# Optimization experiments

Hardware: AMD Instinct MI355X
Metric: run time of the kernel (lower is better)

The kernel has to match this reference:

```python
import jax, jax.numpy as jnp
import numpy as np

EPS = 1e-7  # eps used inside bbox_iou
LAMBDA_BBOX = 1.0
LAMBDA_CLS = 1.0


def _coords(b):
    x, y, w, h = b[..., 0], b[..., 1], b[..., 2], b[..., 3]
    return x - w / 2, y - h / 2, x + w / 2, y + h / 2


def _pairwise_giou_loss(pred, target):
    # pred [B,T,4] -> [B,T,1,4]; target [B,O,4] -> [B,1,O,4]; broadcast to [B,T,O]
    b1x1, b1y1, b1x2, b1y2 = _coords(pred[:, :, None, :])
    b2x1, b2y1, b2x2, b2y2 = _coords(target[:, None, :, :])
    w1, h1 = b1x2 - b1x1, b1y2 - b1y1 + EPS
    w2, h2 = b2x2 - b2x1, b2y2 - b2y1 + EPS
    inter = jnp.clip(jnp.minimum(b1x2, b2x2) - jnp.maximum(b1x1, b2x1), 0) * \
            jnp.clip(jnp.minimum(b1y2, b2y2) - jnp.maximum(b1y1, b2y1), 0)
    union = w1 * h1 + w2 * h2 - inter + EPS
    iou = inter / union
    cw = jnp.maximum(b1x2, b2x2) - jnp.minimum(b1x1, b2x1)
    ch = jnp.maximum(b1y2, b2y2) - jnp.minimum(b1y1, b2y1)
    c_area = cw * ch + EPS
    giou = iou - (c_area - union) / c_area
    return 1.0 - giou  # [B,T,O]


def _lsa_rows(c):
    # Jonker-Volgenant shortest augmenting path (same algorithm as scipy's
    # linear_sum_assignment). c is [n, m] with n <= m; returns col4row [n].
    n, m = c.shape
    u = np.zeros(n)
    v = np.zeros(m)
    col4row = np.full(n, -1, np.int64)
    row4col = np.full(m, -1, np.int64)
    for cur in range(n):
        shortest = np.full(m, np.inf)
        path = np.full(m, -1, np.int64)
        SR = np.zeros(n, bool)
        SC = np.zeros(m, bool)
        min_val = 0.0
        i = cur
        sink = -1
        while sink == -1:
            SR[i] = True
            r = min_val + c[i] - u[i] - v
            upd = (~SC) & (r < shortest)
            shortest[upd] = r[upd]
            path[upd] = i
            masked = np.where(SC, np.inf, shortest)
            j = int(np.argmin(masked))
            min_val = masked[j]
            SC[j] = True
            if row4col[j] == -1:
                sink = j
            else:
                i = row4col[j]
        u[cur] += min_val
        sr = SR.copy(); sr[cur] = False
        u[sr] += min_val - shortest[col4row[sr]]
        v[SC] -= min_val - shortest[SC]
        j = sink
        while True:
            i = path[j]
            row4col[j] = i
            col4row[i], j = j, col4row[i]
            if i == cur:
                break
    return col4row


def _hungarian_np(cost):
    # Host callback; sequential per-batch like the original scipy loop.
    cost = np.asarray(cost, np.float64)
    B, T, O = cost.shape
    pred_idx = np.zeros((B, O), np.int32)
    tgt_idx = np.zeros((B, O), np.int32)
    for b in range(B):
        col4row = _lsa_rows(cost[b].T)  # assign each target (O rows) a token
        order = np.argsort(col4row)      # sort by pred index like scipy output
        pred_idx[b] = col4row[order].astype(np.int32)
        tgt_idx[b] = order.astype(np.int32)
    return pred_idx, tgt_idx


def _cost_matrix(pred_bboxes, target_bboxes, pred_classes, target_classes):
    B, T, C = pred_classes.shape
    O = target_classes.shape[1]
    log_probs = jax.nn.log_softmax(pred_classes, axis=-1)              # [B,T,C]
    idx = jnp.broadcast_to(target_classes[:, None, :], (B, T, O))      # [B,T,O]
    cls_neg_log = -jnp.take_along_axis(log_probs, idx, axis=-1)        # [B,T,O]
    ciou_loss = _pairwise_giou_loss(pred_bboxes, target_bboxes)        # [B,T,O]
    return LAMBDA_BBOX * ciou_loss + LAMBDA_CLS * cls_neg_log


def setup_inputs() -> dict:
    key = jax.random.key(0)
    k1, k2, k3, k4 = jax.random.split(key, 4)
    B, T, O, C = 32, 2048, 128, 80
    return {
        "pred_bboxes": jax.random.uniform(k1, (B, T, 4), dtype=jnp.float32),
        "target_bboxes": jax.random.uniform(k2, (B, O, 4), dtype=jnp.float32),
        "pred_classes": jax.random.normal(k3, (B, T, C), dtype=jnp.float32),
        "target_classes": jax.random.randint(k4, (B, O), 0, C, dtype=jnp.int32),
    }


def reference(pred_bboxes, target_bboxes, pred_classes, target_classes):
    cost = _cost_matrix(pred_bboxes, target_bboxes, pred_classes, target_classes)
    B, _, O = cost.shape
    out_spec = (jax.ShapeDtypeStruct((B, O), jnp.int32),
                jax.ShapeDtypeStruct((B, O), jnp.int32))
    pred_idx, tgt_idx = jax.pure_callback(_hungarian_np, out_spec, cost)
    return pred_idx, tgt_idx
```

## Files before the change

kernel.cpp:

```cpp
#include <hip/hip_runtime.h>
#include <math.h>
#include <float.h>

#define BB 32
#define TT 2048
#define OO 128
#define CC 80
#define EPSF 1e-7f
#define NT 256
#define SLOTS 8
#define CPAD 84

struct alignas(16) URow { double u; int row; int pad; };
struct alignas(8)  P2   { int i; int j; };
struct alignas(16) Cand { double v; int j; int pad; };

template<int CTRL>
__device__ __forceinline__ void dpp_lexmin(double& bv, int& bj) {
    int lo = __double2loint(bv), hi = __double2hiint(bv);
    int tlo = __builtin_amdgcn_update_dpp(0, lo, CTRL, 0xF, 0xF, false);
    int thi = __builtin_amdgcn_update_dpp(0x7FF00000, hi, CTRL, 0xF, 0xF, false);
    int tj  = __builtin_amdgcn_update_dpp(0x7FFFFFFF, bj, CTRL, 0xF, 0xF, false);
    double tv = __hiloint2double(thi, tlo);
    if (tv <= bv) { bv = tv; bj = tj; }
}

__global__ __launch_bounds__(NT) void cost_fused_kernel(
    const float* __restrict__ pb, const float* __restrict__ tb,
    const float* __restrict__ cls, const int* __restrict__ tcls,
    float* __restrict__ cost, unsigned long long* __restrict__ rowminarg) {
#pragma clang fp contract(off)
    int b = blockIdx.y;
    int t0 = blockIdx.x * NT;
    int tid = threadIdx.x;

    __shared__ float s_xv[NT * CPAD];
    __shared__ float s_x1[OO], s_y1[OO], s_x2[OO], s_y2[OO], s_w2h2[OO];
    __shared__ int s_tc[OO];

    const float* cbase = cls + ((size_t)b * TT + t0) * CC;
    #pragma unroll
    for (int k = 0; k < CC / 4; ++k) {
        int idx4 = (k * NT + tid) * 4;
        float4 vv = *(const float4*)(cbase + idx4);
        int r = idx4 / CC;
        int c = idx4 - r * CC;
        *(float4*)(&s_xv[r * CPAD + c]) = vv;
    }
    if (tid < OO) {
        float4 tbox = ((const float4*)tb)[b * OO + tid];
        float x1 = tbox.x - tbox.z / 2.f;
        float y1 = tbox.y - tbox.w / 2.f;
        float x2 = tbox.x + tbox.z / 2.f;
        float y2 = tbox.y + tbox.w / 2.f;
        s_x1[tid] = x1; s_y1[tid] = y1; s_x2[tid] = x2; s_y2[tid] = y2;
        float w2 = x2 - x1;
        float h2 = (y2 - y1) + EPSF;
        s_w2h2[tid] = w2 * h2;
        s_tc[tid] = tcls[b * OO + tid];
    }
    __syncthreads();

    size_t bt = (size_t)b * TT + t0 + tid;
    float4 pbox = ((const float4*)pb)[bt];
    float b1x1 = pbox.x - pbox.z / 2.f;
    float b1y1 = pbox.y - pbox.w / 2.f;
    float b1x2 = pbox.x + pbox.z / 2.f;
    float b1y2 = pbox.y + pbox.w / 2.f;
    float w1 = b1x2 - b1x1;
    float h1 = (b1y2 - b1y1) + EPSF;
    float w1h1 = w1 * h1;

    const float* xr = &s_xv[tid * CPAD];
    float m = xr[0];
    #pragma unroll
    for (int c = 1; c < CC; ++c) m = fmaxf(m, xr[c]);
    float ssum = 0.f;
    #pragma unroll
    for (int c = 0; c < CC; ++c) ssum += expf(xr[c] - m);
    float ls = logf(ssum);

    float* cbt = cost + (size_t)b * OO * TT + t0;
    for (int o = 0; o < OO; ++o) {
        float b2x1 = s_x1[o], b2y1 = s_y1[o], b2x2 = s_x2[o], b2y2 = s_y2[o];
        float iw = fminf(b1x2, b2x2) - fmaxf(b1x1, b2x1);
        float ih = fminf(b1y2, b2y2) - fmaxf(b1y1, b2y1);
        iw = fmaxf(iw, 0.f);
        ih = fmaxf(ih, 0.f);
        float inter = iw * ih;
        float uni = ((w1h1 + s_w2h2[o]) - inter) + EPSF;
        float iou = inter / uni;
        float cw = fmaxf(b1x2, b2x2) - fminf(b1x1, b2x1);
        float ch = fmaxf(b1y2, b2y2) - fminf(b1y1, b2y1);
        float c_area = (cw * ch) + EPSF;
        float giou = iou - (c_area - uni) / c_area;
        float bbox_loss = 1.0f - giou;

        float xc = xr[s_tc[o]];
        float shifted = xc - m;
        float cls_neg = -(shifted - ls);

        float cval = bbox_loss + cls_neg;
        cbt[(size_t)o * TT + tid] = cval;

        unsigned long long kv =
            ((unsigned long long)__float_as_uint(cval) << 32)
            | (unsigned long long)(unsigned)(t0 + tid);
        #pragma unroll
        for (int off = 1; off < 64; off <<= 1) {
            unsigned long long o2 = __shfl_xor(kv, off);
            kv = (o2 < kv) ? o2 : kv;
        }
        if ((tid & 63) == 0) atomicMin(&rowminarg[b * OO + o], kv);
    }
}

__global__ __launch_bounds__(NT) void lsa_kernel(
    const float* __restrict__ cost,
    const unsigned long long* __restrict__ rowminarg,
    int* __restrict__ out) {
#pragma clang fp contract(off)
    int b = blockIdx.x;
    int tid = threadIdx.x;
    int lane = tid & 63;
    int wave = tid >> 6;

    __shared__ URow sh_urow[TT];
    __shared__ P2   sh_path2[TT];
    __shared__ int  sh_row4col[TT];
    __shared__ int  sh_claim[TT];
    __shared__ int  sh_col4row[OO];
    __shared__ double sh_u[OO];
    __shared__ int  sh_amin[OO];
    __shared__ int  sh_flag[OO];
    __shared__ int  sh_freelist[OO];
    __shared__ int  sh_selj[OO + 8];
    __shared__ double sh_selm[OO + 8];
    __shared__ int  sh_selrow[OO + 8];
    __shared__ Cand sh_cand[2][4];
    __shared__ int  sh_nfree;

    const float* cb = cost + (size_t)b * OO * TT;
    const int jbase = tid * SLOTS;

    double v_[SLOTS];
    double key[SLOTS];
    #pragma unroll
    for (int s = 0; s < SLOTS; ++s) v_[s] = 0.0;

    if (tid < OO) {
        unsigned long long kv = rowminarg[b * OO + tid];
        sh_u[tid] = (double)__uint_as_float((unsigned)(kv >> 32));
        sh_amin[tid] = (int)(kv & 0xFFFFFFFFull);
        sh_col4row[tid] = -1;
    }
    for (int j = tid; j < TT; j += NT) { sh_row4col[j] = -1; sh_claim[j] = 0x7FFFFFFF; }
    __syncthreads();

    if (tid < OO) atomicMin(&sh_claim[sh_amin[tid]], tid);
    __syncthreads();
    if (tid < OO) {
        int j = sh_amin[tid];
        if (sh_claim[j] == tid) { sh_col4row[tid] = j; sh_row4col[j] = tid; }
    }
    __syncthreads();

    for (int j = tid; j < TT; j += NT) {
        int r = sh_row4col[j];
        URow t; t.row = r; t.u = (r >= 0) ? sh_u[r] : 0.0; t.pad = 0;
        sh_urow[j] = t;
    }
    if (tid < OO) sh_flag[tid] = (sh_col4row[tid] < 0) ? 1 : 0;
    __syncthreads();
    if (tid < OO && sh_flag[tid]) {
        int rank = 0;
        for (int o = 0; o < tid; ++o) rank += sh_flag[o];
        sh_freelist[rank] = tid;
    }
    if (tid == 0) {
        int nf = 0;
        for (int o = 0; o < OO; ++o) nf += sh_flag[o];
        sh_nfree = nf;
    }
    __syncthreads();
    int nfree = sh_nfree;

    int par = 0;
    for (int fi = 0; fi < nfree; ++fi) {
        int cur = sh_freelist[fi];

        #pragma unroll
        for (int s = 0; s < SLOTS; ++s) key[s] = INFINITY;
        int selbits = 0;
        double mv = 0.0;
        int i = cur, jc = -1;
        double ui = sh_u[cur];
        const float* crow0 = cb + (size_t)i * TT + jbase;
        float4 c0 = *(const float4*)crow0;
        float4 c1 = *(const float4*)(crow0 + 4);
        int L = 0, sink;

        while (true) {
            float cv[SLOTS] = {c0.x, c0.y, c0.z, c0.w, c1.x, c1.y, c1.z, c1.w};

            double bv = INFINITY;
            int bj = TT;
            #pragma unroll
            for (int s = 0; s < SLOTS; ++s) {
                if (!((selbits >> s) & 1)) {
                    double r = ((mv + (double)cv[s]) - ui) - v_[s];
                    if (r < key[s]) {
                        key[s] = r;
                        P2 p; p.i = i; p.j = jc;
                        sh_path2[s * NT + tid] = p;
                    }
                    double kk = key[s];
                    if (kk < bv) { bv = kk; bj = jbase + s; }
                }
            }
            dpp_lexmin<0x111>(bv, bj);
            dpp_lexmin<0x112>(bv, bj);
            dpp_lexmin<0x114>(bv, bj);
            dpp_lexmin<0x118>(bv, bj);
            dpp_lexmin<0x142>(bv, bj);
            dpp_lexmin<0x143>(bv, bj);
            int rlo = __builtin_amdgcn_readlane(__double2loint(bv), 63);
            int rhi = __builtin_amdgcn_readlane(__double2hiint(bv), 63);
            double wv = __hiloint2double(rhi, rlo);
            int wj = __builtin_amdgcn_readlane(bj, 63);

            par ^= 1;
            if (lane == 0) {
                Cand c; c.v = wv; c.j = wj; c.pad = 0;
                sh_cand[par][wave] = c;
            }
            __syncthreads();

            Cand cc = sh_cand[par][0];
            double MV = cc.v; int BJ = cc.j;
            #pragma unroll
            for (int w = 1; w < 4; ++w) {
                Cand c2 = sh_cand[par][w];
                if (c2.v < MV || (c2.v == MV && c2.j < BJ)) { MV = c2.v; BJ = c2.j; }
            }
            mv = MV;
            if ((BJ >> 3) == tid) selbits |= 1 << (BJ & 7);
            if (tid == 0) sh_selj[L] = BJ;

            URow ur = sh_urow[BJ];
            if (ur.row < 0) { sink = BJ; break; }
            if (tid == 0) { sh_selm[L] = MV; sh_selrow[L] = ur.row; }
            i = ur.row; ui = ur.u; jc = BJ;
            L++;
            const float* crow = cb + (size_t)i * TT + jbase;
            c0 = *(const float4*)crow;
            c1 = *(const float4*)(crow + 4);
        }

        double M = mv;
        #pragma unroll
        for (int s = 0; s < SLOTS; ++s)
            if ((selbits >> s) & 1) v_[s] = v_[s] - (M - key[s]);
        for (int k = tid; k < L; k += NT)
            sh_u[sh_selrow[k]] = sh_u[sh_selrow[k]] + (M - sh_selm[k]);
        if (tid == 0) {
            sh_u[cur] = sh_u[cur] + M;
            int j = sink;
            while (true) {
                P2 p = sh_path2[(j & 7) * NT + (j >> 3)];
                int ii = p.i;
                sh_row4col[j] = ii;
                sh_col4row[ii] = j;
                if (ii == cur) break;
                j = p.j;
            }
        }
        __syncthreads();
        if (tid <= L) {
            int j = sh_selj[tid];
            int r = sh_row4col[j];
            URow t; t.u = sh_u[r]; t.row = r; t.pad = 0;
            sh_urow[j] = t;
        }
        __syncthreads();
    }

    if (tid < OO) {
        int my = sh_col4row[tid];
        int rank = 0;
        for (int o = 0; o < OO; ++o) rank += (sh_col4row[o] < my) ? 1 : 0;
        out[(size_t)b * OO + rank] = my;
        out[(size_t)(BB + b) * OO + rank] = tid;
    }
}

extern "C" void kernel_launch(void* const* d_in, const int* in_sizes, int n_in,
                              void* d_out, int out_size, void* d_ws, size_t ws_size,
                              hipStream_t stream) {
    const float* pred_bboxes = (const float*)d_in[0];
    const float* target_bboxes = (const float*)d_in[1];
    const float* pred_classes = (const float*)d_in[2];
    const int* target_classes = (const int*)d_in[3];
    int* out = (int*)d_out;

    float* cost = (float*)d_ws;
    unsigned long long* rowminarg =
        (unsigned long long*)(cost + (size_t)BB * OO * TT);

    hipMemsetAsync(rowminarg, 0xFF, (size_t)BB * OO * 8, stream);

    dim3 cgrid(TT / NT, BB);
    cost_fused_kernel<<<cgrid, NT, 0, stream>>>(pred_bboxes, target_bboxes,
                                                pred_classes, target_classes,
                                                cost, rowminarg);
    lsa_kernel<<<BB, NT, 0, stream>>>(cost, rowminarg, out);
}
```

Baseline: 291.9 us.

## Add auction-style augmenting row reduction before shortest-path LSA and drop atomic rowmin

Adds an augmenting row reduction phase, as in Jonker-Volgenant, that processes free rows from a queue. For each row it finds the best and second-best reduced cost with DPP top-2 reductions, then reassigns the column and lowers its price. The goal is to leave fewer unassigned rows for the expensive sequential shortest-augmenting-path loop. The cost kernel now writes per-tile row minima to a buffer instead of using global atomicMin, which removes the memset launch. The risks are extra barriers per ARR step, capped at 256 steps, and the possibility that the dual variables (u, v) no longer match the later phase's invariants.

Result: slower. 328.0 us (+12.4%).

```diff
diff --git a/kernel.cpp b/kernel.cpp
--- a/kernel.cpp
+++ b/kernel.cpp
@@ -10,10 +10,13 @@
 #define NT 256
 #define SLOTS 8
 #define CPAD 84
+#define NTILE 8
+#define ARR_CAP 256
 
 struct alignas(16) URow { double u; int row; int pad; };
 struct alignas(8)  P2   { int i; int j; };
 struct alignas(16) Cand { double v; int j; int pad; };
+struct alignas(16) A3   { double m1; double m2; int j1; int pad; };
 
 template<int CTRL>
 __device__ __forceinline__ void dpp_lexmin(double& bv, int& bj) {
@@ -25,18 +28,48 @@
     if (tv <= bv) { bv = tv; bj = tj; }
 }
 
+template<int CTRL>
+__device__ __forceinline__ void dpp_lexmin_f32(float& bv, int& bj) {
+    int tlo = __builtin_amdgcn_update_dpp(0x7F800000, __float_as_int(bv), CTRL, 0xF, 0xF, false);
+    int tj  = __builtin_amdgcn_update_dpp(0x7FFFFFFF, bj, CTRL, 0xF, 0xF, false);
+    float tv = __int_as_float(tlo);
+    if (tv < bv || (tv == bv && tj < bj)) { bv = tv; bj = tj; }
+}
+
+template<int CTRL>
+__device__ __forceinline__ void dpp_top2(double& m1, int& j1, double& m2) {
+    int a1lo = __double2loint(m1), a1hi = __double2hiint(m1);
+    int a2lo = __double2loint(m2), a2hi = __double2hiint(m2);
+    int b1lo = __builtin_amdgcn_update_dpp(0, a1lo, CTRL, 0xF, 0xF, false);
+    int b1hi = __builtin_amdgcn_update_dpp(0x7FF00000, a1hi, CTRL, 0xF, 0xF, false);
+    int bj   = __builtin_amdgcn_update_dpp(0x7FFFFFFF, j1, CTRL, 0xF, 0xF, false);
+    int b2lo = __builtin_amdgcn_update_dpp(0, a2lo, CTRL, 0xF, 0xF, false);
+    int b2hi = __builtin_amdgcn_update_dpp(0x7FF00000, a2hi, CTRL, 0xF, 0xF, false);
+    double om1 = __hiloint2double(b1hi, b1lo);
+    double om2 = __hiloint2double(b2hi, b2lo);
+    bool w = (om1 < m1) || (om1 == m1 && bj < j1);
+    double lose1 = w ? m1 : om1;
+    double keep2 = w ? om2 : m2;
+    if (w) { m1 = om1; j1 = bj; }
+    m2 = (lose1 < keep2) ? lose1 : keep2;
+}
+
 __global__ __launch_bounds__(NT) void cost_fused_kernel(
     const float* __restrict__ pb, const float* __restrict__ tb,
     const float* __restrict__ cls, const int* __restrict__ tcls,
-    float* __restrict__ cost, unsigned long long* __restrict__ rowminarg) {
+    float* __restrict__ cost, unsigned long long* __restrict__ rowmins) {
 #pragma clang fp contract(off)
     int b = blockIdx.y;
-    int t0 = blockIdx.x * NT;
+    int tile = blockIdx.x;
+    int t0 = tile * NT;
     int tid = threadIdx.x;
+    int lane = tid & 63;
+    int wave = tid >> 6;
 
     __shared__ float s_xv[NT * CPAD];
     __shared__ float s_x1[OO], s_y1[OO], s_x2[OO], s_y2[OO], s_w2h2[OO];
     __shared__ int s_tc[OO];
+    __shared__ unsigned long long s_rmin[OO * 4];
 
     const float* cbase = cls + ((size_t)b * TT + t0) * CC;
     #pragma unroll
@@ -103,21 +136,33 @@
         float cval = bbox_loss + cls_neg;
         cbt[(size_t)o * TT + tid] = cval;
 
-        unsigned long long kv =
-            ((unsigned long long)__float_as_uint(cval) << 32)
-            | (unsigned long long)(unsigned)(t0 + tid);
-        #pragma unroll
-        for (int off = 1; off < 64; off <<= 1) {
-            unsigned long long o2 = __shfl_xor(kv, off);
-            kv = (o2 < kv) ? o2 : kv;
-        }
-        if ((tid & 63) == 0) atomicMin(&rowminarg[b * OO + o], kv);
+        float bvv = cval;
+        int bjj = t0 + tid;
+        dpp_lexmin_f32<0x111>(bvv, bjj);
+        dpp_lexmin_f32<0x112>(bvv, bjj);
+        dpp_lexmin_f32<0x114>(bvv, bjj);
+        dpp_lexmin_f32<0x118>(bvv, bjj);
+        dpp_lexmin_f32<0x142>(bvv, bjj);
+        dpp_lexmin_f32<0x143>(bvv, bjj);
+        if (lane == 63)
+            s_rmin[o * 4 + wave] =
+                ((unsigned long long)__float_as_uint(bvv) << 32) | (unsigned)bjj;
+    }
+    __syncthreads();
+    if (tid < OO) {
+        unsigned long long r0 = s_rmin[tid * 4 + 0];
+        unsigned long long r1 = s_rmin[tid * 4 + 1];
+        unsigned long long r2 = s_rmin[tid * 4 + 2];
+        unsigned long long r3 = s_rmin[tid * 4 + 3];
+        unsigned long long m01 = r0 < r1 ? r0 : r1;
+        unsigned long long m23 = r2 < r3 ? r2 : r3;
+        rowmins[((size_t)b * NTILE + tile) * OO + tid] = m01 < m23 ? m01 : m23;
     }
 }
 
 __global__ __launch_bounds__(NT) void lsa_kernel(
     const float* __restrict__ cost,
-    const unsigned long long* __restrict__ rowminarg,
+    const unsigned long long* __restrict__ rowmins,
     int* __restrict__ out) {
 #pragma clang fp contract(off)
     int b = blockIdx.x;
@@ -133,12 +178,15 @@
     __shared__ double sh_u[OO];
     __shared__ int  sh_amin[OO];
     __shared__ int  sh_flag[OO];
+    __shared__ int  sh_q[OO + ARR_CAP + 16];
     __shared__ int  sh_freelist[OO];
     __shared__ int  sh_selj[OO + 8];
     __shared__ double sh_selm[OO + 8];
     __shared__ int  sh_selrow[OO + 8];
     __shared__ Cand sh_cand[2][4];
+    __shared__ A3   sh_arr[4];
     __shared__ int  sh_nfree;
+    __shared__ int  sh_qt;
 
     const float* cb = cost + (size_t)b * OO * TT;
     const int jbase = tid * SLOTS;
@@ -149,9 +197,15 @@
     for (int s = 0; s < SLOTS; ++s) v_[s] = 0.0;
 
     if (tid < OO) {
-        unsigned long long kv = rowminarg[b * OO + tid];
-        sh_u[tid] = (double)__uint_as_float((unsigned)(kv >> 32));
-        sh_amin[tid] = (int)(kv & 0xFFFFFFFFull);
+        const unsigned long long* p = rowmins + (size_t)b * NTILE * OO + tid;
+        unsigned long long best = p[0];
+        #pragma unroll
+        for (int t = 1; t < NTILE; ++t) {
+            unsigned long long x = p[t * OO];
+            if (x < best) best = x;
+        }
+        sh_u[tid] = (double)__uint_as_float((unsigned)(best >> 32));
+        sh_amin[tid] = (int)(best & 0xFFFFFFFFull);
         sh_col4row[tid] = -1;
     }
     for (int j = tid; j < TT; j += NT) { sh_row4col[j] = -1; sh_claim[j] = 0x7FFFFFFF; }
@@ -162,8 +216,83 @@
     if (tid < OO) {
         int j = sh_amin[tid];
         if (sh_claim[j] == tid) { sh_col4row[tid] = j; sh_row4col[j] = tid; }
-    }
-    __syncthreads();
+        sh_flag[tid] = (sh_col4row[tid] < 0) ? 1 : 0;
+    }
+    __syncthreads();
+    if (tid < OO && sh_flag[tid]) {
+        int rank = 0;
+        for (int o = 0; o < tid; ++o) rank += sh_flag[o];
+        sh_q[rank] = tid;
+    }
+    if (tid == 0) {
+        int nf = 0;
+        for (int o = 0; o < OO; ++o) nf += sh_flag[o];
+        sh_qt = nf;
+    }
+    __syncthreads();
+
+    int qh = 0, qt = sh_qt, steps = 0;
+    while (qh < qt && steps < ARR_CAP) {
+        int i = sh_q[qh];
+        const float* crow = cb + (size_t)i * TT + jbase;
+        float4 c0 = *(const float4*)crow;
+        float4 c1 = *(const float4*)(crow + 4);
+        float cv[SLOTS] = {c0.x, c0.y, c0.z, c0.w, c1.x, c1.y, c1.z, c1.w};
+        double m1 = INFINITY, m2 = INFINITY;
+        int j1 = 0x7FFFFFFF;
+        #pragma unroll
+        for (int s = 0; s < SLOTS; ++s) {
+            double r = (double)cv[s] - v_[s];
+            bool lt = (r < m1);
+            double lose = lt ? m1 : r;
+            if (lt) { m1 = r; j1 = jbase + s; }
+            if (lose < m2) m2 = lose;
+        }
+        dpp_top2<0x111>(m1, j1, m2);
+        dpp_top2<0x112>(m1, j1, m2);
+        dpp_top2<0x114>(m1, j1, m2);
+        dpp_top2<0x118>(m1, j1, m2);
+        dpp_top2<0x142>(m1, j1, m2);
+        dpp_top2<0x143>(m1, j1, m2);
+        if (lane == 63) { A3 a; a.m1 = m1; a.m2 = m2; a.j1 = j1; a.pad = 0; sh_arr[wave] = a; }
+        __syncthreads();
+
+        A3 a0 = sh_arr[0];
+        double U1 = a0.m1, U2 = a0.m2;
+        int J1 = a0.j1;
+        #pragma unroll
+        for (int w = 1; w < 4; ++w) {
+            A3 aw = sh_arr[w];
+            bool wn = (aw.m1 < U1) || (aw.m1 == U1 && aw.j1 < J1);
+            double lose1 = wn ? U1 : aw.m1;
+            double keep2 = wn ? aw.m2 : U2;
+            if (wn) { U1 = aw.m1; J1 = aw.j1; }
+            U2 = (lose1 < keep2) ? lose1 : keep2;
+        }
+        qh++; steps++;
+        if (U1 < U2) {
+            if ((J1 >> 3) == tid) {
+                double d = U2 - U1;
+                int sl = J1 & 7;
+                #pragma unroll
+                for (int ss = 0; ss < SLOTS; ++ss)
+                    if (ss == sl) v_[ss] = v_[ss] - d;
+            }
+            if (tid == 0) {
+                int k = sh_row4col[J1];
+                sh_row4col[J1] = i;
+                sh_col4row[i] = J1;
+                sh_u[i] = U2;
+                int nqt = qt;
+                if (k >= 0) { sh_col4row[k] = -1; sh_q[qt] = k; nqt = qt + 1; }
+                sh_qt = nqt;
+            }
+        } else {
+            if (tid == 0) sh_qt = qt;
+        }
+        __syncthreads();
+        qt = sh_qt;
+    }
 
     for (int j = tid; j < TT; j += NT) {
         int r = sh_row4col[j];
@@ -304,14 +433,12 @@
     int* out = (int*)d_out;
 
     float* cost = (float*)d_ws;
-    unsigned long long* rowminarg =
+    unsigned long long* rowmins =
         (unsigned long long*)(cost + (size_t)BB * OO * TT);
 
-    hipMemsetAsync(rowminarg, 0xFF, (size_t)BB * OO * 8, stream);
-
-    dim3 cgrid(TT / NT, BB);
+    dim3 cgrid(NTILE, BB);
     cost_fused_kernel<<<cgrid, NT, 0, stream>>>(pred_bboxes, target_bboxes,
                                                 pred_classes, target_classes,
-                                                cost, rowminarg);
-    lsa_kernel<<<BB, NT, 0, stream>>>(cost, rowminarg, out);
-}
+                                                cost, rowmins);
+    lsa_kernel<<<BB, NT, 0, stream>>>(cost, rowmins, out);
+}
```

## Fuse cost and assignment kernels with per-batch arrival counter handoff

Applied to the files above, without the earlier changes.

Merges the cost-matrix kernel and the Hungarian solver into one launch. Tile-0 blocks spin on a per-batch atomic counter until all eight tiles of that batch have written their cost slices, then run the assignment solver. Row-min reduction now uses float DPP plus a shared-memory combine and writes per-tile minima instead of 64-bit global atomicMin, which removes the memset of the rowmin buffer. The goal is to save a launch boundary and let early batches start solving while others are still computing. The spin-wait depends on all producer blocks being scheduled and adds a shared-memory union sized by the larger phase.

Result: no change. 295.6 us (+1.3%).

```diff
diff --git a/kernel.cpp b/kernel.cpp
--- a/kernel.cpp
+++ b/kernel.cpp
@@ -10,6 +10,7 @@
 #define NT 256
 #define SLOTS 8
 #define CPAD 84
+#define NTILE 8
 
 struct alignas(16) URow { double u; int row; int pad; };
 struct alignas(8)  P2   { int i; int j; };
@@ -25,120 +26,159 @@
     if (tv <= bv) { bv = tv; bj = tj; }
 }
 
-__global__ __launch_bounds__(NT) void cost_fused_kernel(
+template<int CTRL>
+__device__ __forceinline__ void dpp_lexmin_f32(float& bv, int& bj) {
+    int tlo = __builtin_amdgcn_update_dpp(0x7F800000, __float_as_int(bv), CTRL, 0xF, 0xF, false);
+    int tj  = __builtin_amdgcn_update_dpp(0x7FFFFFFF, bj, CTRL, 0xF, 0xF, false);
+    float tv = __int_as_float(tlo);
+    if (tv < bv || (tv == bv && tj < bj)) { bv = tv; bj = tj; }
+}
+
+union SM {
+    struct {
+        float xv[NT * CPAD];
+        float x1[OO], y1[OO], x2[OO], y2[OO], w2h2[OO];
+        int   tc[OO];
+        unsigned long long rmin[OO * 4];
+    } c;
+    struct {
+        URow   urow[TT];
+        P2     path2[TT];
+        int    row4col[TT];
+        int    claim[TT];
+        int    col4row[OO];
+        double u[OO];
+        int    amin[OO];
+        int    flag[OO];
+        int    freelist[OO];
+        int    selj[OO + 8];
+        double selm[OO + 8];
+        int    selrow[OO + 8];
+        Cand   cand[2][4];
+        int    nfree;
+    } l;
+};
+
+__global__ __launch_bounds__(NT) void hung_fused_kernel(
     const float* __restrict__ pb, const float* __restrict__ tb,
     const float* __restrict__ cls, const int* __restrict__ tcls,
-    float* __restrict__ cost, unsigned long long* __restrict__ rowminarg) {
+    float* __restrict__ cost, unsigned long long* __restrict__ rowmins,
+    int* __restrict__ cnt, int* __restrict__ out) {
 #pragma clang fp contract(off)
-    int b = blockIdx.y;
-    int t0 = blockIdx.x * NT;
-    int tid = threadIdx.x;
-
-    __shared__ float s_xv[NT * CPAD];
-    __shared__ float s_x1[OO], s_y1[OO], s_x2[OO], s_y2[OO], s_w2h2[OO];
-    __shared__ int s_tc[OO];
-
-    const float* cbase = cls + ((size_t)b * TT + t0) * CC;
-    #pragma unroll
-    for (int k = 0; k < CC / 4; ++k) {
-        int idx4 = (k * NT + tid) * 4;
-        float4 vv = *(const float4*)(cbase + idx4);
-        int r = idx4 / CC;
-        int c = idx4 - r * CC;
-        *(float4*)(&s_xv[r * CPAD + c]) = vv;
-    }
-    if (tid < OO) {
-        float4 tbox = ((const float4*)tb)[b * OO + tid];
-        float x1 = tbox.x - tbox.z / 2.f;
-        float y1 = tbox.y - tbox.w / 2.f;
-        float x2 = tbox.x + tbox.z / 2.f;
-        float y2 = tbox.y + tbox.w / 2.f;
-        s_x1[tid] = x1; s_y1[tid] = y1; s_x2[tid] = x2; s_y2[tid] = y2;
-        float w2 = x2 - x1;
-        float h2 = (y2 - y1) + EPSF;
-        s_w2h2[tid] = w2 * h2;
-        s_tc[tid] = tcls[b * OO + tid];
-    }
-    __syncthreads();
-
-    size_t bt = (size_t)b * TT + t0 + tid;
-    float4 pbox = ((const float4*)pb)[bt];
-    float b1x1 = pbox.x - pbox.z / 2.f;
-    float b1y1 = pbox.y - pbox.w / 2.f;
-    float b1x2 = pbox.x + pbox.z / 2.f;
-    float b1y2 = pbox.y + pbox.w / 2.f;
-    float w1 = b1x2 - b1x1;
-    float h1 = (b1y2 - b1y1) + EPSF;
-    float w1h1 = w1 * h1;
-
-    const float* xr = &s_xv[tid * CPAD];
-    float m = xr[0];
-    #pragma unroll
-    for (int c = 1; c < CC; ++c) m = fmaxf(m, xr[c]);
-    float ssum = 0.f;
-    #pragma unroll
-    for (int c = 0; c < CC; ++c) ssum += expf(xr[c] - m);
-    float ls = logf(ssum);
-
-    float* cbt = cost + (size_t)b * OO * TT + t0;
-    for (int o = 0; o < OO; ++o) {
-        float b2x1 = s_x1[o], b2y1 = s_y1[o], b2x2 = s_x2[o], b2y2 = s_y2[o];
-        float iw = fminf(b1x2, b2x2) - fmaxf(b1x1, b2x1);
-        float ih = fminf(b1y2, b2y2) - fmaxf(b1y1, b2y1);
-        iw = fmaxf(iw, 0.f);
-        ih = fmaxf(ih, 0.f);
-        float inter = iw * ih;
-        float uni = ((w1h1 + s_w2h2[o]) - inter) + EPSF;
-        float iou = inter / uni;
-        float cw = fmaxf(b1x2, b2x2) - fminf(b1x1, b2x1);
-        float ch = fmaxf(b1y2, b2y2) - fminf(b1y1, b2y1);
-        float c_area = (cw * ch) + EPSF;
-        float giou = iou - (c_area - uni) / c_area;
-        float bbox_loss = 1.0f - giou;
-
-        float xc = xr[s_tc[o]];
-        float shifted = xc - m;
-        float cls_neg = -(shifted - ls);
-
-        float cval = bbox_loss + cls_neg;
-        cbt[(size_t)o * TT + tid] = cval;
-
-        unsigned long long kv =
-            ((unsigned long long)__float_as_uint(cval) << 32)
-            | (unsigned long long)(unsigned)(t0 + tid);
-        #pragma unroll
-        for (int off = 1; off < 64; off <<= 1) {
-            unsigned long long o2 = __shfl_xor(kv, off);
-            kv = (o2 < kv) ? o2 : kv;
-        }
-        if ((tid & 63) == 0) atomicMin(&rowminarg[b * OO + o], kv);
-    }
-}
-
-__global__ __launch_bounds__(NT) void lsa_kernel(
-    const float* __restrict__ cost,
-    const unsigned long long* __restrict__ rowminarg,
-    int* __restrict__ out) {
-#pragma clang fp contract(off)
-    int b = blockIdx.x;
+    __shared__ SM sm;
+
+    int bx = blockIdx.x;
+    int b = bx >> 3;
+    int tile = bx & 7;
+    int t0 = tile * NT;
     int tid = threadIdx.x;
     int lane = tid & 63;
     int wave = tid >> 6;
 
-    __shared__ URow sh_urow[TT];
-    __shared__ P2   sh_path2[TT];
-    __shared__ int  sh_row4col[TT];
-    __shared__ int  sh_claim[TT];
-    __shared__ int  sh_col4row[OO];
-    __shared__ double sh_u[OO];
-    __shared__ int  sh_amin[OO];
-    __shared__ int  sh_flag[OO];
-    __shared__ int  sh_freelist[OO];
-    __shared__ int  sh_selj[OO + 8];
-    __shared__ double sh_selm[OO + 8];
-    __shared__ int  sh_selrow[OO + 8];
-    __shared__ Cand sh_cand[2][4];
-    __shared__ int  sh_nfree;
+    {
+        const float* cbase = cls + ((size_t)b * TT + t0) * CC;
+        #pragma unroll
+        for (int k = 0; k < CC / 4; ++k) {
+            int idx4 = (k * NT + tid) * 4;
+            float4 vv = *(const float4*)(cbase + idx4);
+            int r = idx4 / CC;
+            int c = idx4 - r * CC;
+            *(float4*)(&sm.c.xv[r * CPAD + c]) = vv;
+        }
+        if (tid < OO) {
+            float4 tbox = ((const float4*)tb)[b * OO + tid];
+            float x1 = tbox.x - tbox.z / 2.f;
+            float y1 = tbox.y - tbox.w / 2.f;
+            float x2 = tbox.x + tbox.z / 2.f;
+            float y2 = tbox.y + tbox.w / 2.f;
+            sm.c.x1[tid] = x1; sm.c.y1[tid] = y1;
+            sm.c.x2[tid] = x2; sm.c.y2[tid] = y2;
+            float w2 = x2 - x1;
+            float h2 = (y2 - y1) + EPSF;
+            sm.c.w2h2[tid] = w2 * h2;
+            sm.c.tc[tid] = tcls[b * OO + tid];
+        }
+        __syncthreads();
+
+        size_t bt = (size_t)b * TT + t0 + tid;
+        float4 pbox = ((const float4*)pb)[bt];
+        float b1x1 = pbox.x - pbox.z / 2.f;
+        float b1y1 = pbox.y - pbox.w / 2.f;
+        float b1x2 = pbox.x + pbox.z / 2.f;
+        float b1y2 = pbox.y + pbox.w / 2.f;
+        float w1 = b1x2 - b1x1;
+        float h1 = (b1y2 - b1y1) + EPSF;
+        float w1h1 = w1 * h1;
+
+        const float* xr = &sm.c.xv[tid * CPAD];
+        float m = xr[0];
+        #pragma unroll
+        for (int c = 1; c < CC; ++c) m = fmaxf(m, xr[c]);
+        float ssum = 0.f;
+        #pragma unroll
+        for (int c = 0; c < CC; ++c) ssum += expf(xr[c] - m);
+        float ls = logf(ssum);
+
+        float* cbt = cost + (size_t)b * OO * TT + t0;
+        for (int o = 0; o < OO; ++o) {
+            float b2x1 = sm.c.x1[o], b2y1 = sm.c.y1[o];
+            float b2x2 = sm.c.x2[o], b2y2 = sm.c.y2[o];
+            float iw = fminf(b1x2, b2x2) - fmaxf(b1x1, b2x1);
+            float ih = fminf(b1y2, b2y2) - fmaxf(b1y1, b2y1);
+            iw = fmaxf(iw, 0.f);
+            ih = fmaxf(ih, 0.f);
+            float inter = iw * ih;
+            float uni = ((w1h1 + sm.c.w2h2[o]) - inter) + EPSF;
+            float iou = inter / uni;
+            float cw = fmaxf(b1x2, b2x2) - fminf(b1x1, b2x1);
+            float ch = fmaxf(b1y2, b2y2) - fminf(b1y1, b2y1);
+            float c_area = (cw * ch) + EPSF;
+            float giou = iou - (c_area - uni) / c_area;
+            float bbox_loss = 1.0f - giou;
+
+            float xc = xr[sm.c.tc[o]];
+            float shifted = xc - m;
+            float cls_neg = -(shifted - ls);
+
+            float cval = bbox_loss + cls_neg;
+            cbt[(size_t)o * TT + tid] = cval;
+
+            float bvv = cval;
+            int bjj = t0 + tid;
+            dpp_lexmin_f32<0x111>(bvv, bjj);
+            dpp_lexmin_f32<0x112>(bvv, bjj);
+            dpp_lexmin_f32<0x114>(bvv, bjj);
+            dpp_lexmin_f32<0x118>(bvv, bjj);
+            dpp_lexmin_f32<0x142>(bvv, bjj);
+            dpp_lexmin_f32<0x143>(bvv, bjj);
+            if (lane == 63)
+                sm.c.rmin[o * 4 + wave] =
+                    ((unsigned long long)__float_as_uint(bvv) << 32) | (unsigned)bjj;
+        }
+        __syncthreads();
+        if (tid < OO) {
+            unsigned long long r0 = sm.c.rmin[tid * 4 + 0];
+            unsigned long long r1 = sm.c.rmin[tid * 4 + 1];
+            unsigned long long r2 = sm.c.rmin[tid * 4 + 2];
+            unsigned long long r3 = sm.c.rmin[tid * 4 + 3];
+            unsigned long long m01 = r0 < r1 ? r0 : r1;
+            unsigned long long m23 = r2 < r3 ? r2 : r3;
+            rowmins[((size_t)b * NTILE + tile) * OO + tid] = m01 < m23 ? m01 : m23;
+        }
+        __syncthreads();
+        if (tid == 0)
+            __hip_atomic_fetch_add(&cnt[b], 1, __ATOMIC_RELEASE,
+                                   __HIP_MEMORY_SCOPE_AGENT);
+    }
+
+    if (tile != 0) return;
+
+    if (tid == 0) {
+        while (__hip_atomic_load(&cnt[b], __ATOMIC_ACQUIRE,
+                                 __HIP_MEMORY_SCOPE_AGENT) < NTILE)
+            __builtin_amdgcn_s_sleep(2);
+    }
+    __syncthreads();
 
     const float* cb = cost + (size_t)b * OO * TT;
     const int jbase = tid * SLOTS;
@@ -149,52 +189,58 @@
     for (int s = 0; s < SLOTS; ++s) v_[s] = 0.0;
 
     if (tid < OO) {
-        unsigned long long kv = rowminarg[b * OO + tid];
-        sh_u[tid] = (double)__uint_as_float((unsigned)(kv >> 32));
-        sh_amin[tid] = (int)(kv & 0xFFFFFFFFull);
-        sh_col4row[tid] = -1;
-    }
-    for (int j = tid; j < TT; j += NT) { sh_row4col[j] = -1; sh_claim[j] = 0x7FFFFFFF; }
-    __syncthreads();
-
-    if (tid < OO) atomicMin(&sh_claim[sh_amin[tid]], tid);
+        const unsigned long long* p = rowmins + (size_t)b * NTILE * OO + tid;
+        unsigned long long best = p[0];
+        #pragma unroll
+        for (int t = 1; t < NTILE; ++t) {
+            unsigned long long x = p[t * OO];
+            if (x < best) best = x;
+        }
+        sm.l.u[tid] = (double)__uint_as_float((unsigned)(best >> 32));
+        sm.l.amin[tid] = (int)(best & 0xFFFFFFFFull);
+        sm.l.col4row[tid] = -1;
+    }
+    for (int j = tid; j < TT; j += NT) { sm.l.row4col[j] = -1; sm.l.claim[j] = 0x7FFFFFFF; }
+    __syncthreads();
+
+    if (tid < OO) atomicMin(&sm.l.claim[sm.l.amin[tid]], tid);
     __syncthreads();
     if (tid < OO) {
-        int j = sh_amin[tid];
-        if (sh_claim[j] == tid) { sh_col4row[tid] = j; sh_row4col[j] = tid; }
+        int j = sm.l.amin[tid];
+        if (sm.l.claim[j] == tid) { sm.l.col4row[tid] = j; sm.l.row4col[j] = tid; }
     }
     __syncthreads();
 
     for (int j = tid; j < TT; j += NT) {
-        int r = sh_row4col[j];
-        URow t; t.row = r; t.u = (r >= 0) ? sh_u[r] : 0.0; t.pad = 0;
-        sh_urow[j] = t;
-    }
-    if (tid < OO) sh_flag[tid] = (sh_col4row[tid] < 0) ? 1 : 0;
-    __syncthreads();
-    if (tid < OO && sh_flag[tid]) {
+        int r = sm.l.row4col[j];
+        URow t; t.row = r; t.u = (r >= 0) ? sm.l.u[r] : 0.0; t.pad = 0;
+        sm.l.urow[j] = t;
+    }
+    if (tid < OO) sm.l.flag[tid] = (sm.l.col4row[tid] < 0) ? 1 : 0;
+    __syncthreads();
+    if (tid < OO && sm.l.flag[tid]) {
         int rank = 0;
-        for (int o = 0; o < tid; ++o) rank += sh_flag[o];
-        sh_freelist[rank] = tid;
+        for (int o = 0; o < tid; ++o) rank += sm.l.flag[o];
+        sm.l.freelist[rank] = tid;
     }
     if (tid == 0) {
         int nf = 0;
-        for (int o = 0; o < OO; ++o) nf += sh_flag[o];
-        sh_nfree = nf;
-    }
-    __syncthreads();
-    int nfree = sh_nfree;
+        for (int o = 0; o < OO; ++o) nf += sm.l.flag[o];
+        sm.l.nfree = nf;
+    }
+    __syncthreads();
+    int nfree = sm.l.nfree;
 
     int par = 0;
     for (int fi = 0; fi < nfree; ++fi) {
-        int cur = sh_freelist[fi];
+        int cur = sm.l.freelist[fi];
 
         #pragma unroll
         for (int s = 0; s < SLOTS; ++s) key[s] = INFINITY;
         int selbits = 0;
         double mv = 0.0;
         int i = cur, jc = -1;
-        double ui = sh_u[cur];
+        double ui = sm.l.u[cur];
         const float* crow0 = cb + (size_t)i * TT + jbase;
         float4 c0 = *(const float4*)crow0;
         float4 c1 = *(const float4*)(crow0 + 4);
@@ -212,7 +258,7 @@
                     if (r < key[s]) {
                         key[s] = r;
                         P2 p; p.i = i; p.j = jc;
-                        sh_path2[s * NT + tid] = p;
+                        sm.l.path2[s * NT + tid] = p;
                     }
                     double kk = key[s];
                     if (kk < bv) { bv = kk; bj = jbase + s; }
@@ -232,24 +278,24 @@
             par ^= 1;
             if (lane == 0) {
                 Cand c; c.v = wv; c.j = wj; c.pad = 0;
-                sh_cand[par][wave] = c;
+                sm.l.cand[par][wave] = c;
             }
             __syncthreads();
 
-            Cand cc = sh_cand[par][0];
+            Cand cc = sm.l.cand[par][0];
             double MV = cc.v; int BJ = cc.j;
             #pragma unroll
             for (int w = 1; w < 4; ++w) {
-                Cand c2 = sh_cand[par][w];
+                Cand c2 = sm.l.cand[par][w];
                 if (c2.v < MV || (c2.v == MV && c2.j < BJ)) { MV = c2.v; BJ = c2.j; }
             }
             mv = MV;
             if ((BJ >> 3) == tid) selbits |= 1 << (BJ & 7);
-            if (tid == 0) sh_selj[L] = BJ;
-
-            URow ur = sh_urow[BJ];
+            if (tid == 0) sm.l.selj[L] = BJ;
+
+            URow ur = sm.l.urow[BJ];
             if (ur.row < 0) { sink = BJ; break; }
-            if (tid == 0) { sh_selm[L] = MV; sh_selrow[L] = ur.row; }
+            if (tid == 0) { sm.l.selm[L] = MV; sm.l.selrow[L] = ur.row; }
             i = ur.row; ui = ur.u; jc = BJ;
             L++;
             const float* crow = cb + (size_t)i * TT + jbase;
@@ -262,33 +308,33 @@
         for (int s = 0; s < SLOTS; ++s)
             if ((selbits >> s) & 1) v_[s] = v_[s] - (M - key[s]);
         for (int k = tid; k < L; k += NT)
-            sh_u[sh_selrow[k]] = sh_u[sh_selrow[k]] + (M - sh_selm[k]);
+            sm.l.u[sm.l.selrow[k]] = sm.l.u[sm.l.selrow[k]] + (M - sm.l.selm[k]);
         if (tid == 0) {
-            sh_u[cur] = sh_u[cur] + M;
+            sm.l.u[cur] = sm.l.u[cur] + M;
             int j = sink;
             while (true) {
-                P2 p = sh_path2[(j & 7) * NT + (j >> 3)];
+                P2 p = sm.l.path2[(j & 7) * NT + (j >> 3)];
                 int ii = p.i;
-                sh_row4col[j] = ii;
-                sh_col4row[ii] = j;
+                sm.l.row4col[j] = ii;
+                sm.l.col4row[ii] = j;
                 if (ii == cur) break;
                 j = p.j;
             }
         }
         __syncthreads();
         if (tid <= L) {
-            int j = sh_selj[tid];
-            int r = sh_row4col[j];
-            URow t; t.u = sh_u[r]; t.row = r; t.pad = 0;
-            sh_urow[j] = t;
+            int j = sm.l.selj[tid];
+            int r = sm.l.row4col[j];
+            URow t; t.u = sm.l.u[r]; t.row = r; t.pad = 0;
+            sm.l.urow[j] = t;
         }
         __syncthreads();
     }
 
     if (tid < OO) {
-        int my = sh_col4row[tid];
+        int my = sm.l.col4row[tid];
         int rank = 0;
-        for (int o = 0; o < OO; ++o) rank += (sh_col4row[o] < my) ? 1 : 0;
+        for (int o = 0; o < OO; ++o) rank += (sm.l.col4row[o] < my) ? 1 : 0;
         out[(size_t)b * OO + rank] = my;
         out[(size_t)(BB + b) * OO + rank] = tid;
     }
@@ -304,14 +350,13 @@
     int* out = (int*)d_out;
 
     float* cost = (float*)d_ws;
-    unsigned long long* rowminarg =
+    unsigned long long* rowmins =
         (unsigned long long*)(cost + (size_t)BB * OO * TT);
-
-    hipMemsetAsync(rowminarg, 0xFF, (size_t)BB * OO * 8, stream);
-
-    dim3 cgrid(TT / NT, BB);
-    cost_fused_kernel<<<cgrid, NT, 0, stream>>>(pred_bboxes, target_bboxes,
-                                                pred_classes, target_classes,
-                                                cost, rowminarg);
-    lsa_kernel<<<BB, NT, 0, stream>>>(cost, rowminarg, out);
+    int* cnt = (int*)(rowmins + (size_t)BB * NTILE * OO);
+
+    hipMemsetAsync(cnt, 0, BB * sizeof(int), stream);
+
+    hung_fused_kernel<<<BB * NTILE, NT, 0, stream>>>(
+        pred_bboxes, target_bboxes, pred_classes, target_classes,
+        cost, rowmins, cnt, out);
 }
```
